# Kernel tuning notes

Measured on AMD Instinct MI355X. Metric: run time of the kernel, lower is better.

## Reference

```python
import jax, jax.numpy as jnp
import numpy as np

NUM_HEADS = 8
KERNEL = 7  # odd, dilation = 1


def _neighbor_indices(n, k):
    # NATTEN semantics: window start clamped so the kxk window stays inside [0, n)
    r = k // 2
    starts = jnp.clip(jnp.arange(n) - r, 0, n - k)  # [n]
    return starts[:, None] + jnp.arange(k)[None, :]  # [n, k]


def setup_inputs() -> dict:
    key = jax.random.key(0)
    k1, k2, k3, k4 = jax.random.split(key, 4)
    B, H, W, C = 2, 56, 56, 256
    return {
        "x": jax.random.normal(k1, (B, H, W, C), dtype=jnp.float32),
        "w_qk": jax.random.normal(k2, (2 * C, C), dtype=jnp.float32) * 0.02,
        "w_v": jax.random.normal(k3, (C, C), dtype=jnp.float32) * 0.02,
        "w_proj": jax.random.normal(k4, (C, C), dtype=jnp.float32) * 0.02,
        "b_proj": jnp.zeros((C,), dtype=jnp.float32),
    }


def reference(x, w_qk, w_v, w_proj, b_proj):
    B, H, W, C = x.shape
    NH, K = NUM_HEADS, KERNEL
    HD = C // NH
    scale = HD ** -0.5

    # qk / v projections (torch Linear: y = x @ W.T)
    qk = (x @ w_qk.T).reshape(B, H, W, 2, NH, HD)
    q = jnp.moveaxis(qk[:, :, :, 0], 3, 1) * scale  # [B, NH, H, W, HD]
    k = jnp.moveaxis(qk[:, :, :, 1], 3, 1)          # [B, NH, H, W, HD]
    v = jnp.moveaxis((x @ w_v.T).reshape(B, H, W, NH, HD), 3, 1)  # [B, NH, H, W, HD]

    idx_h = _neighbor_indices(H, K)  # [H, K]
    idx_w = _neighbor_indices(W, K)  # [W, K]
    ih = idx_h[:, None, :, None]  # [H, 1, K, 1]
    iw = idx_w[None, :, None, :]  # [1, W, 1, K]

    # Gather per-pixel neighborhoods: [B, NH, H, W, K, K, HD]
    k_nb = k[:, :, ih, iw, :]
    v_nb = v[:, :, ih, iw, :]

    # windowed QK^T -> [B, NH, H, W, K*K]
    attn = jnp.einsum('bnijf,bnijpqf->bnijpq', q, k_nb).reshape(B, NH, H, W, K * K)
    attn = jax.nn.softmax(attn, axis=-1)

    # windowed AV -> [B, NH, H, W, HD]
    out = jnp.einsum('bnijk,bnijkf->bnijf', attn, v_nb.reshape(B, NH, H, W, K * K, HD))

    out = jnp.moveaxis(out, 1, 3).reshape(B, H, W, C)
    out = out @ w_proj.T + b_proj
    return out, attn
```

## Files before the change

kernel.cpp:

```cpp
#include <hip/hip_runtime.h>
#include <math.h>

#define Bb   2
#define Hh   56
#define Ww   56
#define Cc   256
#define NHh  8
#define HDd  32
#define KK   7
#define HWsz (Hh*Ww)
#define Mtot (Bb*Hh*Ww)

typedef __bf16 bf16x8 __attribute__((ext_vector_type(8)));
typedef float  f32x4  __attribute__((ext_vector_type(4)));

__global__ __launch_bounds__(256) void gemm_bf16(
    const float* __restrict__ A, const float* __restrict__ W0,
    const float* __restrict__ W1, float* __restrict__ Cout,
    int Kdim, int N, int n_split, int scale_below, float scale,
    const float* __restrict__ bias)
{
    __shared__ __bf16 As[4096];
    __shared__ __bf16 Bs[4096];

    const int tid = threadIdx.x;
    const int m0  = blockIdx.y * 64;
    const int n0  = blockIdx.x * 64;

    const int mm = tid >> 2;
    const int q  = tid & 3;
    const float* arow = A + (size_t)(m0 + mm) * Kdim + q * 16;
    const int n_idx = n0 + mm;
    const float* brow = (n_idx < n_split ? W0 + (size_t)n_idx * Kdim
                                         : W1 + (size_t)(n_idx - n_split) * Kdim) + q * 16;

    const int ks_st  = q >> 1;
    const int sub_st = mm >> 4;
    const int row_st = mm & 15;
    const int c0_st  = (q & 1) * 2;
    const int blk_st = ks_st * 4 + sub_st;
    const int off0 = blk_st * 512 + row_st * 32 + ((c0_st ^ (row_st & 3)) * 8);
    const int off1 = blk_st * 512 + row_st * 32 + (((c0_st + 1) ^ (row_st & 3)) * 8);

    const int w    = tid >> 6;
    const int lane = tid & 63;
    const int fr_row = lane & 15;
    const int fr_c   = lane >> 4;
    const int fr_off = fr_row * 32 + ((fr_c ^ (fr_row & 3)) * 8);

    f32x4 acc[4] = {};

    for (int k0 = 0; k0 < Kdim; k0 += 64) {
        float4 a0 = *(const float4*)(arow + k0);
        float4 a1 = *(const float4*)(arow + k0 + 4);
        float4 a2 = *(const float4*)(arow + k0 + 8);
        float4 a3 = *(const float4*)(arow + k0 + 12);
        float4 b0 = *(const float4*)(brow + k0);
        float4 b1 = *(const float4*)(brow + k0 + 4);
        float4 b2 = *(const float4*)(brow + k0 + 8);
        float4 b3 = *(const float4*)(brow + k0 + 12);
        __syncthreads();
        bf16x8 av0 = { (__bf16)a0.x, (__bf16)a0.y, (__bf16)a0.z, (__bf16)a0.w,
                       (__bf16)a1.x, (__bf16)a1.y, (__bf16)a1.z, (__bf16)a1.w };
        bf16x8 av1 = { (__bf16)a2.x, (__bf16)a2.y, (__bf16)a2.z, (__bf16)a2.w,
                       (__bf16)a3.x, (__bf16)a3.y, (__bf16)a3.z, (__bf16)a3.w };
        bf16x8 bv0 = { (__bf16)b0.x, (__bf16)b0.y, (__bf16)b0.z, (__bf16)b0.w,
                       (__bf16)b1.x, (__bf16)b1.y, (__bf16)b1.z, (__bf16)b1.w };
        bf16x8 bv1 = { (__bf16)b2.x, (__bf16)b2.y, (__bf16)b2.z, (__bf16)b2.w,
                       (__bf16)b3.x, (__bf16)b3.y, (__bf16)b3.z, (__bf16)b3.w };
        *(bf16x8*)&As[off0] = av0;
        *(bf16x8*)&As[off1] = av1;
        *(bf16x8*)&Bs[off0] = bv0;
        *(bf16x8*)&Bs[off1] = bv1;
        __syncthreads();
        #pragma unroll
        for (int ks = 0; ks < 2; ++ks) {
            bf16x8 af = *(const bf16x8*)&As[(ks * 4 + w) * 512 + fr_off];
            #pragma unroll
            for (int n = 0; n < 4; ++n) {
                bf16x8 bfr = *(const bf16x8*)&Bs[(ks * 4 + n) * 512 + fr_off];
                acc[n] = __builtin_amdgcn_mfma_f32_16x16x32_bf16(af, bfr, acc[n], 0, 0, 0);
            }
        }
    }

    #pragma unroll
    for (int n = 0; n < 4; ++n) {
        const int gcol = n0 + n * 16 + fr_row;
        const float sc_ = (gcol < scale_below) ? scale : 1.f;
        const float bs_ = bias ? bias[gcol] : 0.f;
        #pragma unroll
        for (int r = 0; r < 4; ++r) {
            const int grow = m0 + w * 16 + fr_c * 4 + r;
            Cout[(size_t)grow * N + gcol] = acc[n][r] * sc_ + bs_;
        }
    }
}

__global__ __launch_bounds__(256) void nattn_tiled(
    const float* __restrict__ qkv, float* __restrict__ attn_out,
    float* __restrict__ attn_glob)
{
    __shared__ float Ks[196 * 36];
    __shared__ float Ss[64 * 50];

    const int bx   = blockIdx.x;
    const int head = bx & 7;
    int tq = bx >> 3;
    const int tj = tq % 7; tq /= 7;
    const int ti = tq % 7;
    const int b  = tq / 7;

    const int tid = threadIdx.x;

    int base_h = ti * 8 - 3; if (base_h < 0) base_h = 0; if (base_h > Hh - 14) base_h = Hh - 14;
    int base_w = tj * 8 - 3; if (base_w < 0) base_w = 0; if (base_w > Ww - 14) base_w = Ww - 14;

    const int pixb = b * HWsz;
    const int hoff = head * 32;

    for (int idx = tid; idx < 196 * 8; idx += 256) {
        const int p = idx >> 3, c = idx & 7;
        const int pix = pixb + (base_h + p / 14) * Ww + base_w + p % 14;
        *(float4*)&Ks[p * 36 + c * 4] =
            *(const float4*)&qkv[(size_t)pix * 768 + 256 + hoff + c * 4];
    }
    for (int idx = tid; idx < 64 * 8; idx += 256) {
        const int qq = idx >> 3, c = idx & 7;
        const int pix = pixb + (ti * 8 + (qq >> 3)) * Ww + tj * 8 + (qq & 7);
        *(float4*)&Ss[qq * 36 + c * 4] =
            *(const float4*)&qkv[(size_t)pix * 768 + hoff + c * 4];
    }
    __syncthreads();

    const int q  = tid >> 2;
    const int r  = tid & 3;
    const int qi = ti * 8 + (q >> 3);
    const int qj = tj * 8 + (q & 7);
    int ih0 = qi - 3; if (ih0 < 0) ih0 = 0; if (ih0 > Hh - 7) ih0 = Hh - 7;
    int iw0 = qj - 3; if (iw0 < 0) iw0 = 0; if (iw0 > Ww - 7) iw0 = Ww - 7;
    const int lh0 = ih0 - base_h, lw0 = iw0 - base_w;

    float4 qreg[8];
    #pragma unroll
    for (int c = 0; c < 8; ++c) qreg[c] = *(const float4*)&Ss[q * 36 + c * 4];
    __syncthreads();

    float sc[13];
    float mx = -1e30f;
    #pragma unroll
    for (int tt = 0; tt < 13; ++tt) {
        const int k = r + 4 * tt;
        if (k < 49) {
            const int krow = (lh0 + k / 7) * 14 + lw0 + k % 7;
            const float* kp = &Ks[krow * 36];
            float acc = 0.f;
            #pragma unroll
            for (int c = 0; c < 8; ++c) {
                const float4 kv = *(const float4*)(kp + c * 4);
                acc += qreg[c].x * kv.x + qreg[c].y * kv.y
                     + qreg[c].z * kv.z + qreg[c].w * kv.w;
            }
            sc[tt] = acc;
            mx = fmaxf(mx, acc);
        }
    }
    mx = fmaxf(mx, __shfl_xor(mx, 1));
    mx = fmaxf(mx, __shfl_xor(mx, 2));
    float sum = 0.f;
    #pragma unroll
    for (int tt = 0; tt < 13; ++tt) {
        const int k = r + 4 * tt;
        if (k < 49) { sc[tt] = __expf(sc[tt] - mx); sum += sc[tt]; }
    }
    sum += __shfl_xor(sum, 1);
    sum += __shfl_xor(sum, 2);
    const float inv = 1.f / sum;
    #pragma unroll
    for (int tt = 0; tt < 13; ++tt) {
        const int k = r + 4 * tt;
        if (k < 49) Ss[q * 50 + k] = sc[tt] * inv;
    }
    __syncthreads();

    for (int idx = tid; idx < 196 * 8; idx += 256) {
        const int p = idx >> 3, c = idx & 7;
        const int pix = pixb + (base_h + p / 14) * Ww + base_w + p % 14;
        *(float4*)&Ks[p * 36 + c * 4] =
            *(const float4*)&qkv[(size_t)pix * 768 + 512 + hoff + c * 4];
    }
    const size_t agbase = (size_t)(b * NHh + head) * HWsz;
    for (int idx = tid; idx < 64 * 49; idx += 256) {
        const int qq = idx / 49, k = idx - qq * 49;
        attn_glob[(agbase + (ti * 8 + (qq >> 3)) * Ww + tj * 8 + (qq & 7)) * 49 + k]
            = Ss[qq * 50 + k];
    }
    __syncthreads();

    const int d0 = r * 8;
    float4 a0 = {0, 0, 0, 0}, a1 = {0, 0, 0, 0};
    #pragma unroll
    for (int k = 0; k < 49; ++k) {
        const float pr = Ss[q * 50 + k];
        const int vrow = (lh0 + k / 7) * 14 + lw0 + k % 7;
        const float4 v0 = *(const float4*)&Ks[vrow * 36 + d0];
        const float4 v1 = *(const float4*)&Ks[vrow * 36 + d0 + 4];
        a0.x += pr * v0.x; a0.y += pr * v0.y; a0.z += pr * v0.z; a0.w += pr * v0.w;
        a1.x += pr * v1.x; a1.y += pr * v1.y; a1.z += pr * v1.z; a1.w += pr * v1.w;
    }
    float* op = attn_out + (size_t)(pixb + qi * Ww + qj) * 256 + hoff + d0;
    *(float4*)op = a0;
    *(float4*)(op + 4) = a1;
}

extern "C" void kernel_launch(void* const* d_in, const int* in_sizes, int n_in,
                              void* d_out, int out_size, void* d_ws, size_t ws_size,
                              hipStream_t stream)
{
    const float* x      = (const float*)d_in[0];
    const float* w_qk   = (const float*)d_in[1];
    const float* w_v    = (const float*)d_in[2];
    const float* w_proj = (const float*)d_in[3];
    const float* b_proj = (const float*)d_in[4];

    float* out       = (float*)d_out;
    float* attn_glob = out + (size_t)Mtot * Cc;

    float* qkv_ws  = (float*)d_ws;
    float* attn_ws = qkv_ws + (size_t)Mtot * 768;

    const float scale = 0.17677669529663687f;

    gemm_bf16<<<dim3(768 / 64, Mtot / 64), 256, 0, stream>>>(
        x, w_qk, w_v, qkv_ws, Cc, 768, 512, 256, scale, nullptr);

    nattn_tiled<<<Bb * 7 * 7 * NHh, 256, 0, stream>>>(qkv_ws, attn_ws, attn_glob);

    gemm_bf16<<<dim3(256 / 64, Mtot / 64), 256, 0, stream>>>(
        attn_ws, w_proj, w_proj, out, Cc, Cc, 1 << 30, 0, 1.f, b_proj);
}
```

Baseline: 115.8 us.

## Shrink attention tiles to 8x4 queries with 8 threads per query and V prefetch

The neighborhood attention kernel now uses 8x4 query tiles instead of 8x8, which doubles the block count and shrinks the K/V halo tile to 14x10. Each query gets 8 threads instead of 4, and Q is loaded straight from global memory into registers. V is prefetched into registers during the QK/softmax phase, so only the register-to-LDS store remains after the barrier, and launch bounds are set for 5 blocks per CU. The aim is more parallelism, smaller LDS per block and hidden V load latency. The cost is a larger relative halo overhead per tile (140 loaded rows for 32 queries versus 196 for 64) and more register pressure.

```diff
diff --git a/kernel.cpp b/kernel.cpp
--- a/kernel.cpp
+++ b/kernel.cpp
@@ -97,62 +97,73 @@
     }
 }
 
-__global__ __launch_bounds__(256) void nattn_tiled(
+__global__ __launch_bounds__(256, 5) void nattn_84(
     const float* __restrict__ qkv, float* __restrict__ attn_out,
     float* __restrict__ attn_glob)
 {
-    __shared__ float Ks[196 * 36];
-    __shared__ float Ss[64 * 50];
+    __shared__ float Ks[140 * 36];
+    __shared__ float Ss[32 * 49];
 
     const int bx   = blockIdx.x;
     const int head = bx & 7;
-    int tq = bx >> 3;
-    const int tj = tq % 7; tq /= 7;
-    const int ti = tq % 7;
-    const int b  = tq / 7;
-
+    int t = bx >> 3;
+    const int tj = t % 14; t /= 14;
+    const int ti = t % 7;
+    const int b  = t / 7;
     const int tid = threadIdx.x;
 
     int base_h = ti * 8 - 3; if (base_h < 0) base_h = 0; if (base_h > Hh - 14) base_h = Hh - 14;
-    int base_w = tj * 8 - 3; if (base_w < 0) base_w = 0; if (base_w > Ww - 14) base_w = Ww - 14;
+    int base_w = tj * 4 - 3; if (base_w < 0) base_w = 0; if (base_w > Ww - 10) base_w = Ww - 10;
 
     const int pixb = b * HWsz;
     const int hoff = head * 32;
 
-    for (int idx = tid; idx < 196 * 8; idx += 256) {
-        const int p = idx >> 3, c = idx & 7;
-        const int pix = pixb + (base_h + p / 14) * Ww + base_w + p % 14;
-        *(float4*)&Ks[p * 36 + c * 4] =
-            *(const float4*)&qkv[(size_t)pix * 768 + 256 + hoff + c * 4];
-    }
-    for (int idx = tid; idx < 64 * 8; idx += 256) {
-        const int qq = idx >> 3, c = idx & 7;
-        const int pix = pixb + (ti * 8 + (qq >> 3)) * Ww + tj * 8 + (qq & 7);
-        *(float4*)&Ss[qq * 36 + c * 4] =
-            *(const float4*)&qkv[(size_t)pix * 768 + hoff + c * 4];
+    #pragma unroll
+    for (int it = 0; it < 5; ++it) {
+        const int idx = tid + it * 256;
+        if (idx < 1120) {
+            const int p = idx >> 3, c = idx & 7;
+            const int pix = pixb + (base_h + p / 10) * Ww + base_w + p % 10;
+            *(float4*)&Ks[p * 36 + c * 4] =
+                *(const float4*)&qkv[(size_t)pix * 768 + 256 + hoff + c * 4];
+        }
+    }
+
+    const int q  = tid >> 3;
+    const int r  = tid & 7;
+    const int qi = ti * 8 + (q >> 2);
+    const int qj = tj * 4 + (q & 3);
+
+    float4 qreg[8];
+    {
+        const float* qp = &qkv[(size_t)(pixb + qi * Ww + qj) * 768 + hoff];
+        #pragma unroll
+        for (int c = 0; c < 8; ++c) qreg[c] = *(const float4*)(qp + c * 4);
+    }
+
+    float4 vreg[5];
+    #pragma unroll
+    for (int it = 0; it < 5; ++it) {
+        const int idx = tid + it * 256;
+        if (idx < 1120) {
+            const int p = idx >> 3, c = idx & 7;
+            const int pix = pixb + (base_h + p / 10) * Ww + base_w + p % 10;
+            vreg[it] = *(const float4*)&qkv[(size_t)pix * 768 + 512 + hoff + c * 4];
+        }
     }
     __syncthreads();
 
-    const int q  = tid >> 2;
-    const int r  = tid & 3;
-    const int qi = ti * 8 + (q >> 3);
-    const int qj = tj * 8 + (q & 7);
     int ih0 = qi - 3; if (ih0 < 0) ih0 = 0; if (ih0 > Hh - 7) ih0 = Hh - 7;
     int iw0 = qj - 3; if (iw0 < 0) iw0 = 0; if (iw0 > Ww - 7) iw0 = Ww - 7;
     const int lh0 = ih0 - base_h, lw0 = iw0 - base_w;
 
-    float4 qreg[8];
-    #pragma unroll
-    for (int c = 0; c < 8; ++c) qreg[c] = *(const float4*)&Ss[q * 36 + c * 4];
-    __syncthreads();
-
-    float sc[13];
+    float sc[7];
     float mx = -1e30f;
     #pragma unroll
-    for (int tt = 0; tt < 13; ++tt) {
-        const int k = r + 4 * tt;
+    for (int tt = 0; tt < 7; ++tt) {
+        const int k = r + 8 * tt;
         if (k < 49) {
-            const int krow = (lh0 + k / 7) * 14 + lw0 + k % 7;
+            const int krow = (lh0 + k / 7) * 10 + lw0 + k % 7;
             const float* kp = &Ks[krow * 36];
             float acc = 0.f;
             #pragma unroll
@@ -167,50 +178,51 @@
     }
     mx = fmaxf(mx, __shfl_xor(mx, 1));
     mx = fmaxf(mx, __shfl_xor(mx, 2));
+    mx = fmaxf(mx, __shfl_xor(mx, 4));
     float sum = 0.f;
     #pragma unroll
-    for (int tt = 0; tt < 13; ++tt) {
-        const int k = r + 4 * tt;
+    for (int tt = 0; tt < 7; ++tt) {
+        const int k = r + 8 * tt;
         if (k < 49) { sc[tt] = __expf(sc[tt] - mx); sum += sc[tt]; }
     }
     sum += __shfl_xor(sum, 1);
     sum += __shfl_xor(sum, 2);
+    sum += __shfl_xor(sum, 4);
     const float inv = 1.f / sum;
     #pragma unroll
-    for (int tt = 0; tt < 13; ++tt) {
-        const int k = r + 4 * tt;
-        if (k < 49) Ss[q * 50 + k] = sc[tt] * inv;
+    for (int tt = 0; tt < 7; ++tt) {
+        const int k = r + 8 * tt;
+        if (k < 49) Ss[q * 49 + k] = sc[tt] * inv;
     }
     __syncthreads();
 
-    for (int idx = tid; idx < 196 * 8; idx += 256) {
-        const int p = idx >> 3, c = idx & 7;
-        const int pix = pixb + (base_h + p / 14) * Ww + base_w + p % 14;
-        *(float4*)&Ks[p * 36 + c * 4] =
-            *(const float4*)&qkv[(size_t)pix * 768 + 512 + hoff + c * 4];
+    #pragma unroll
+    for (int it = 0; it < 5; ++it) {
+        const int idx = tid + it * 256;
+        if (idx < 1120) {
+            const int p = idx >> 3, c = idx & 7;
+            *(float4*)&Ks[p * 36 + c * 4] = vreg[it];
+        }
     }
     const size_t agbase = (size_t)(b * NHh + head) * HWsz;
-    for (int idx = tid; idx < 64 * 49; idx += 256) {
+    for (int idx = tid; idx < 32 * 49; idx += 256) {
         const int qq = idx / 49, k = idx - qq * 49;
-        attn_glob[(agbase + (ti * 8 + (qq >> 3)) * Ww + tj * 8 + (qq & 7)) * 49 + k]
-            = Ss[qq * 50 + k];
+        attn_glob[(agbase + (ti * 8 + (qq >> 2)) * Ww + tj * 4 + (qq & 3)) * 49 + k]
+            = Ss[qq * 49 + k];
     }
     __syncthreads();
 
-    const int d0 = r * 8;
-    float4 a0 = {0, 0, 0, 0}, a1 = {0, 0, 0, 0};
+    const int d0 = r * 4;
+    float4 a0 = {0, 0, 0, 0};
     #pragma unroll
     for (int k = 0; k < 49; ++k) {
-        const float pr = Ss[q * 50 + k];
-        const int vrow = (lh0 + k / 7) * 14 + lw0 + k % 7;
+        const float pr = Ss[q * 49 + k];
+        const int vrow = (lh0 + k / 7) * 10 + lw0 + k % 7;
         const float4 v0 = *(const float4*)&Ks[vrow * 36 + d0];
-        const float4 v1 = *(const float4*)&Ks[vrow * 36 + d0 + 4];
         a0.x += pr * v0.x; a0.y += pr * v0.y; a0.z += pr * v0.z; a0.w += pr * v0.w;
-        a1.x += pr * v1.x; a1.y += pr * v1.y; a1.z += pr * v1.z; a1.w += pr * v1.w;
     }
     float* op = attn_out + (size_t)(pixb + qi * Ww + qj) * 256 + hoff + d0;
     *(float4*)op = a0;
-    *(float4*)(op + 4) = a1;
 }
 
 extern "C" void kernel_launch(void* const* d_in, const int* in_sizes, int n_in,
@@ -234,7 +246,7 @@
     gemm_bf16<<<dim3(768 / 64, Mtot / 64), 256, 0, stream>>>(
         x, w_qk, w_v, qkv_ws, Cc, 768, 512, 256, scale, nullptr);
 
-    nattn_tiled<<<Bb * 7 * 7 * NHh, 256, 0, stream>>>(qkv_ws, attn_ws, attn_glob);
+    nattn_84<<<Bb * 7 * 14 * NHh, 256, 0, stream>>>(qkv_ws, attn_ws, attn_glob);
 
     gemm_bf16<<<dim3(256 / 64, Mtot / 64), 256, 0, stream>>>(
         attn_ws, w_proj, w_proj, out, Cc, Cc, 1 << 30, 0, 1.f, b_proj);
```

Result: no change. 117.9 us (+1.8%).
